# Kernel tuning notes

Measured on AMD Instinct MI355X. Metric: run time of the kernel, lower is better.

Reference implementation:

```python
import jax, jax.numpy as jnp
import numpy as np
from jax import lax

COND, PRED, DH, NOUT = 64, 32, 128, 1
M, LQ, N, LR = 8, 256, 64, 512


def setup_inputs() -> dict:
    key = jax.random.key(0)
    ks = jax.random.split(key, 8)
    g = lambda k, sh, s=0.05: jax.random.normal(k, sh, jnp.float32) * s
    return {
        "query": jax.random.normal(ks[0], (M, LQ), jnp.float32),
        "ref": jax.random.normal(ks[1], (N, LR), jnp.float32),
        "q_weight": g(ks[2], (DH, 1, COND)),
        "q_bias": jnp.zeros((DH,), jnp.float32),
        "k_weight": g(ks[3], (DH, 1, COND)),
        "k_bias": jnp.zeros((DH,), jnp.float32),
        "v_weight": g(ks[4], (DH, 1, PRED), 0.1),
        "v_bias": jnp.zeros((DH,), jnp.float32),
        "m_weight": jnp.full((NOUT, 1, COND), 1.0 / COND, jnp.float32),
        "m_bias": jnp.zeros((NOUT,), jnp.float32),
        "o_weight": g(ks[5], (NOUT * PRED, DH), 0.1),
        "o_bias": jnp.zeros((NOUT * PRED,), jnp.float32),
        "m_key": g(ks[6], (1, 1, DH), 1.0),
    }


DN = ('NCH', 'OIH', 'NCH')


def _minmax_conv(x, w, b, offset=None, scale=None):
    # x: [B,1,L], w: [H,1,k] -> y: [B,H,W]. Each length-k window is min-max
    # normalized before the conv contraction. Since offset/scale are constant
    # per window: conv((x-off)/sc) = (conv(x) - off*sum(w)) / sc.
    k = w.shape[-1]
    if offset is None:
        offset = lax.reduce_window(x, jnp.inf, lax.min, (1, 1, k), (1, 1, 1), 'VALID')
    if scale is None:
        mx = lax.reduce_window(x, -jnp.inf, lax.max, (1, 1, k), (1, 1, 1), 'VALID')
        scale = mx - offset
        scale = jnp.where(scale == 0.0, 1.0, scale)
    raw = lax.conv_general_dilated(x, w, (1,), 'VALID', dimension_numbers=DN)
    wsum = w.sum(axis=(1, 2))
    y = (raw - offset * wsum[None, :, None]) / scale + b[None, :, None]
    return y, offset, scale


def reference(query, ref, q_weight, q_bias, k_weight, k_bias, v_weight, v_bias,
              m_weight, m_bias, o_weight, o_bias, m_key):
    cond, pred = q_weight.shape[-1], v_weight.shape[-1]
    # ---- query encoding ----
    q_in = jnp.cumsum(query, axis=1)[:, None, :]
    q, q_off, q_scale = _minmax_conv(q_in, q_weight, q_bias)
    q = q.transpose(0, 2, 1)                   # [M,Q,H]
    Qn = q.shape[1]
    q_scale_t = q_scale.transpose(0, 2, 1)     # [M,Q,1]
    qp = jnp.pad(query, ((0, 0), (cond - 1, 0)))[:, None, :]
    mc = lax.conv_general_dilated(qp, m_weight, (1,), 'VALID', dimension_numbers=DN)
    mc = mc + m_bias[None, :, None]
    mc = mc[..., cond - pred:]                 # [M,NOUT,Q+pred-1]
    widx = jnp.arange(pred)[:, None] + jnp.arange(Qn)[None, :]
    mwin = mc[..., widx]                       # [M,NOUT,pred,Q]
    m = mwin.reshape(mwin.shape[0], -1, Qn).transpose(0, 2, 1)  # [M,Q,NOUT*pred]
    m = m / q_scale_t
    # ---- key / value encoding ----
    k_in = jnp.cumsum(ref, axis=1)[:, None, :-pred]
    k, k_off, k_scale = _minmax_conv(k_in, k_weight, k_bias)
    k = k.transpose(0, 2, 1)                   # [N,K,H]
    v_in = ref[:, None, cond:]
    v, _, _ = _minmax_conv(v_in, v_weight, v_bias,
                           offset=jnp.zeros_like(k_off), scale=k_scale)
    v = v.transpose(0, 2, 1)                   # [N,K,H]
    # ---- scores ----
    full_score = jnp.einsum('mqh,nkh->mqkn', q, k)           # [M,Q,K,N]
    m_score = jnp.sum(q * m_key, axis=-1, keepdims=True)     # [M,Q,1]
    # ---- semi-hard attention: top-1 window per reference series ----
    ref_score = full_score.max(axis=2)         # [M,Q,N]
    max_idx = full_score.argmax(axis=2)        # [M,Q,N]
    n_ids = jnp.arange(v.shape[0])[None, None, :]
    sel_v = v[n_ids, max_idx]                  # [M,Q,N,H]
    sel_v = sel_v @ o_weight.T + o_bias        # [M,Q,N,D]
    scores = jax.nn.softmax(jnp.concatenate([ref_score, m_score], axis=-1), axis=-1)
    rs, ms = scores[..., :-1], scores[..., -1:]
    p = jnp.einsum('mqn,mqnd->mqd', rs, sel_v) + ms * m      # [M,Q,D]
    return p * q_scale_t
```

## Files before the change

### kernel.cpp

```cpp
#include <hip/hip_runtime.h>
#include <cmath>

#define M_B   8
#define LQ    256
#define N_B   64
#define LR    512
#define COND  64
#define PRED  32
#define DH    128
#define QN    193
#define KN    417
#define QPAD  256
#define KPAD  448

typedef _Float16 half8 __attribute__((ext_vector_type(8)));
typedef float f32x16 __attribute__((ext_vector_type(16)));

__device__ __forceinline__ f32x16 mfma_f16(half8 a, half8 b, f32x16 c) {
    return __builtin_amdgcn_mfma_f32_32x32x16_f16(a, b, c, 0, 0, 0);
}
__device__ __forceinline__ f32x16 zero16() {
    f32x16 z;
    #pragma unroll
    for (int i = 0; i < 16; i++) z[i] = 0.f;
    return z;
}

#define GLOAD_LDS16(g, l) __builtin_amdgcn_global_load_lds( \
    (const __attribute__((address_space(1))) void*)(g), \
    (__attribute__((address_space(3))) void*)(l), 16, 0, 0)

__global__ void k0_scan(const float* __restrict__ q, const float* __restrict__ r,
                        float* cs_q, float* cs_r, float* mc,
                        float* q_off, float* q_scale, float* k_off, float* k_scale,
                        const float* __restrict__ mw, const float* __restrict__ mb) {
    __shared__ float x[512];
    __shared__ float s[512];
    __shared__ float P[256];
    int b = blockIdx.x, t = threadIdx.x;
    if (b < M_B) {
        x[t] = q[b * 256 + t];
        __syncthreads();
        s[t] = x[t];
        __syncthreads();
        for (int off = 1; off < 256; off <<= 1) {
            float v = (t >= off) ? s[t - off] : 0.f;
            __syncthreads();
            s[t] += v;
            __syncthreads();
        }
        cs_q[b * 256 + t] = s[t];
        float acc = mb[0];
        for (int j = 0; j < 64; j++) {
            int qi = t + j - 63;
            if (qi >= 0) acc += mw[j] * x[qi];
        }
        mc[b * 256 + t] = acc;
        if (t < QN) {
            float mn = s[t], mx = s[t];
            for (int j = 1; j < 64; j++) {
                float v = s[t + j];
                mn = fminf(mn, v); mx = fmaxf(mx, v);
            }
            float sc = mx - mn; if (sc == 0.f) sc = 1.f;
            q_off[b * QPAD + t] = mn;
            q_scale[b * QPAD + t] = sc;
        } else {
            q_off[b * QPAD + t] = 0.f;
            q_scale[b * QPAD + t] = 1.f;
        }
    } else {
        int n = b - M_B;
        x[t] = r[n * 512 + t];
        x[t + 256] = r[n * 512 + t + 256];
        __syncthreads();
        P[t] = x[2 * t] + x[2 * t + 1];
        __syncthreads();
        for (int off = 1; off < 256; off <<= 1) {
            float v = (t >= off) ? P[t - off] : 0.f;
            __syncthreads();
            P[t] += v;
            __syncthreads();
        }
        s[2 * t + 1] = P[t];
        s[2 * t]     = P[t] - x[2 * t + 1];
        __syncthreads();
        cs_r[n * 512 + t] = s[t];
        cs_r[n * 512 + t + 256] = s[t + 256];
        for (int p = t; p < KPAD; p += 256) {
            if (p < KN) {
                float mn = s[p], mx = s[p];
                for (int j = 1; j < 64; j++) {
                    float v = s[p + j];
                    mn = fminf(mn, v); mx = fmaxf(mx, v);
                }
                float sc = mx - mn; if (sc == 0.f) sc = 1.f;
                k_off[n * KPAD + p] = mn;
                k_scale[n * KPAD + p] = sc;
            } else {
                k_off[n * KPAD + p] = 0.f;
                k_scale[n * KPAD + p] = 1.f;
            }
        }
    }
}

__global__ void k1_qfeat(const float* __restrict__ cs_q, const float* __restrict__ q_off,
                         const float* __restrict__ q_scale,
                         const float* __restrict__ qw, const float* __restrict__ qb,
                         float* qfeat, _Float16* qg) {
    __shared__ float w[128 * 65];
    __shared__ float wsum[128];
    __shared__ float csS[80];
    __shared__ float offS[16], sclS[16];
    int m = blockIdx.x, chunk = blockIdx.y, t = threadIdx.x;
    int qbase = chunk * 16;
    for (int i = t; i < 8192; i += 256) {
        int h = i >> 6, j = i & 63;
        w[h * 65 + j] = qw[i];
    }
    if (t < 80) {
        int ci = qbase + t;
        csS[t] = (ci < 256) ? cs_q[m * 256 + ci] : 0.f;
    }
    if (t < 16) {
        int qpos = qbase + t;
        if (qpos < QN) { offS[t] = q_off[m * QPAD + qpos]; sclS[t] = q_scale[m * QPAD + qpos]; }
        else { offS[t] = 0.f; sclS[t] = 1.f; }
    }
    __syncthreads();
    if (t < 128) {
        float sm = 0.f;
        for (int j = 0; j < 64; j++) sm += w[t * 65 + j];
        wsum[t] = sm;
    }
    __syncthreads();
    int h = t & 127, ql0 = t >> 7;
    float bias = qb[h];
    int c = h >> 4, kh = (h >> 3) & 1, j5 = h & 7;
    for (int ql = ql0; ql < 16; ql += 2) {
        int qpos = qbase + ql;
        float val = 0.f;
        if (qpos < QN) {
            float raw = 0.f;
            #pragma unroll 8
            for (int j = 0; j < 64; j++) raw += w[h * 65 + j] * csS[ql + j];
            val = (raw - offS[ql] * wsum[h]) / sclS[ql] + bias;
        }
        qfeat[((size_t)m * QPAD + qpos) * 128 + h] = val;
        _Float16 hi = (_Float16)val;
        _Float16 lo = (_Float16)((val - (float)hi) * 1024.0f);
        int wv = (qpos >> 6) & 3, rr = (qpos >> 5) & 1, lr_ = qpos & 31;
        size_t fb = ((size_t)(m * 4 + wv) * 32) + (size_t)(rr * 8 + c) * 2;
        size_t li = (size_t)(kh * 32 + lr_) * 8 + j5;
        qg[fb * 512 + li] = hi;
        qg[(fb + 1) * 512 + li] = lo;
    }
}

__global__ void k2_kv(const float* __restrict__ cs_r, const float* __restrict__ ref,
                      const float* __restrict__ k_off, const float* __restrict__ k_scale,
                      const float* __restrict__ kw, const float* __restrict__ kb,
                      const float* __restrict__ vw, const float* __restrict__ vb,
                      _Float16* kg, float* vfeat) {
    __shared__ float w[128 * 65];
    __shared__ float vwS[128 * 33];
    __shared__ float wsum[128];
    __shared__ float csS[128];
    __shared__ float refS[96];
    __shared__ float koS[64], ksS[64];
    int n = blockIdx.x, chunk = blockIdx.y, t = threadIdx.x;
    int kbase = chunk * 64;
    for (int i = t; i < 8192; i += 256) { int h = i >> 6, j = i & 63; w[h * 65 + j] = kw[i]; }
    for (int i = t; i < 4096; i += 256) { int h = i >> 5, j = i & 31; vwS[h * 33 + j] = vw[i]; }
    if (t < 128) { int ci = kbase + t; csS[t] = (ci < 512) ? cs_r[n * 512 + ci] : 0.f; }
    if (t < 96)  { int ri = 64 + kbase + t; refS[t] = (ri < 512) ? ref[n * 512 + ri] : 0.f; }
    if (t < 64) {
        int kp = kbase + t;
        if (kp < KN) { koS[t] = k_off[n * KPAD + kp]; ksS[t] = k_scale[n * KPAD + kp]; }
        else { koS[t] = 0.f; ksS[t] = 1.f; }
    }
    __syncthreads();
    if (t < 128) {
        float sm = 0.f;
        for (int j = 0; j < 64; j++) sm += w[t * 65 + j];
        wsum[t] = sm;
    }
    __syncthreads();
    int h = t & 127, kl0 = t >> 7;
    float kbia = kb[h], vbia = vb[h];
    int cb = h >> 3, j5 = h & 7;
    for (int kl = kl0; kl < 64; kl += 2) {
        int kp = kbase + kl;
        float kval = 0.f, vval = 0.f;
        if (kp < KN) {
            float kraw = 0.f;
            #pragma unroll 8
            for (int j = 0; j < 64; j++) kraw += w[h * 65 + j] * csS[kl + j];
            float vraw = 0.f;
            #pragma unroll 8
            for (int j = 0; j < 32; j++) vraw += vwS[h * 33 + j] * refS[kl + j];
            float inv = 1.f / ksS[kl];
            kval = (kraw - koS[kl] * wsum[h]) * inv + kbia;
            vval = vraw * inv + vbia;
        }
        _Float16 khi = (_Float16)kval;
        _Float16 klo = (_Float16)((kval - (float)khi) * 1024.0f);
        size_t rowb = ((size_t)n * KPAD + kp) * 256;
        int sw = kp & 31;
        kg[rowb + (size_t)((cb ^ sw) * 8) + j5] = khi;
        kg[rowb + (size_t)(((16 + cb) ^ sw) * 8) + j5] = klo;
        vfeat[((size_t)n * KPAD + kp) * 128 + h] = vval;
    }
}

__launch_bounds__(256, 2)
__global__ void k3_score(const _Float16* __restrict__ qg, const _Float16* __restrict__ kg,
                         float* __restrict__ bscore, int* __restrict__ bidx) {
    __shared__ _Float16 Kbuf[2][32 * 256];
    const int blk = blockIdx.x;
    const int n = blk & 63, qt = blk >> 6;
    const int t = threadIdx.x, w = t >> 6, l = t & 63;
    const int lrow = l & 31, khalf = l >> 5;

    half8 qf[2][8][2];
    {
        const half8* qb = (const half8*)qg + (size_t)(qt * 4 + w) * 32 * 64 + l;
        #pragma unroll
        for (int r = 0; r < 2; r++)
            #pragma unroll
            for (int c = 0; c < 8; c++)
                #pragma unroll
                for (int h = 0; h < 2; h++)
                    qf[r][c][h] = qb[((r * 8 + c) * 2 + h) * 64];
    }

    const _Float16* ksrc = kg + (size_t)n * KPAD * 256;

    float best[2][16];
    unsigned bkt[4] = {0u, 0u, 0u, 0u};
    #pragma unroll
    for (int r = 0; r < 2; r++)
        #pragma unroll
        for (int g = 0; g < 16; g++) best[r][g] = -INFINITY;

    #pragma unroll
    for (int rd = 0; rd < 4; rd++) {
        int e = (rd * 4 + w) * 512 + l * 8;
        GLOAD_LDS16(ksrc + e, &Kbuf[0][0] + e);
    }

    for (int kt = 0; kt < 14; kt++) {
        __syncthreads();
        if (kt < 13) {
            const _Float16* src = ksrc + (size_t)(kt + 1) * (32 * 256);
            _Float16* dst = &Kbuf[(kt + 1) & 1][0];
            #pragma unroll
            for (int rd = 0; rd < 4; rd++) {
                int e = (rd * 4 + w) * 512 + l * 8;
                GLOAD_LDS16(src + e, dst + e);
            }
        }
        const _Float16* kb = &Kbuf[kt & 1][0];
        f32x16 accH[2], accL[2];
        accH[0] = zero16(); accH[1] = zero16();
        accL[0] = zero16(); accL[1] = zero16();
        #pragma unroll
        for (int c = 0; c < 8; c++) {
            half8 bh = *(const half8*)(kb + lrow * 256 + (((c * 2 + khalf) ^ lrow) * 8));
            half8 bl = *(const half8*)(kb + lrow * 256 + (((16 + c * 2 + khalf) ^ lrow) * 8));
            #pragma unroll
            for (int r = 0; r < 2; r++) {
                accH[r] = mfma_f16(qf[r][c][0], bh, accH[r]);
                accL[r] = mfma_f16(qf[r][c][0], bl, accL[r]);
                accL[r] = mfma_f16(qf[r][c][1], bh, accL[r]);
            }
        }
        const int kp = kt * 32 + lrow;
        const bool valid = kp < KN;
        #pragma unroll
        for (int r = 0; r < 2; r++) {
            #pragma unroll
            for (int g = 0; g < 16; g++) {
                float s = accH[r][g] + accL[r][g] * (1.0f / 1024.0f);
                if (valid && (s > best[r][g])) {
                    best[r][g] = s;
                    const int slot = r * 16 + g;
                    const unsigned sh = (unsigned)(slot & 7) * 4u;
                    bkt[slot >> 3] = (bkt[slot >> 3] & ~(0xFu << sh)) | ((unsigned)kt << sh);
                }
            }
        }
    }

    #pragma unroll
    for (int r = 0; r < 2; r++) {
        #pragma unroll
        for (int g = 0; g < 16; g++) {
            float s = best[r][g];
            const int slot = r * 16 + g;
            int ktb = (int)((bkt[slot >> 3] >> ((slot & 7) * 4)) & 0xFu);
            int kp = ktb * 32 + lrow;
            for (int msk = 1; msk < 32; msk <<= 1) {
                float os = __shfl_xor(s, msk, 64);
                int okp = __shfl_xor(kp, msk, 64);
                if (os > s || (os == s && okp < kp)) { s = os; kp = okp; }
            }
            if (lrow == 0) {
                int row = (g & 3) + 8 * (g >> 2) + 4 * khalf;
                int mq = qt * 256 + w * 64 + r * 32 + row;
                if ((mq & 255) < QN) {
                    bscore[(size_t)mq * 64 + n] = s;
                    bidx[(size_t)mq * 64 + n] = kp;
                }
            }
        }
    }
}

__global__ void k4_out(const float* __restrict__ qfeat, const float* __restrict__ vfeat,
                       const float* __restrict__ bscore, const int* __restrict__ bidx,
                       const float* __restrict__ q_scale, const float* __restrict__ mc,
                       const float* __restrict__ mkey,
                       const float* __restrict__ ow, const float* __restrict__ ob,
                       float* out) {
    __shared__ float sL[64]; __shared__ int iL[64];
    __shared__ float rsL[64];
    __shared__ float redA[128];
    __shared__ float wL[128];
    int bid = blockIdx.x, t = threadIdx.x;
    int m = bid / QN, qpos = bid - m * QN;
    int mq = m * QPAD + qpos;
    if (t < 64) { sL[t] = bscore[(size_t)mq * 64 + t]; iL[t] = bidx[(size_t)mq * 64 + t]; }
    redA[t] = qfeat[(size_t)mq * 128 + t] * mkey[t];
    __syncthreads();
    for (int off = 64; off > 0; off >>= 1) {
        if (t < off) redA[t] += redA[t + off];
        __syncthreads();
    }
    float msv = redA[0];
    __syncthreads();
    redA[t] = (t < 64) ? sL[t] : -INFINITY;
    __syncthreads();
    for (int off = 64; off > 0; off >>= 1) {
        if (t < off) redA[t] = fmaxf(redA[t], redA[t + off]);
        __syncthreads();
    }
    float mx = fmaxf(redA[0], msv);
    __syncthreads();
    float e = (t < 64) ? expf(sL[t] - mx) : 0.f;
    redA[t] = e;
    if (t < 64) rsL[t] = e;
    __syncthreads();
    for (int off = 64; off > 0; off >>= 1) {
        if (t < off) redA[t] += redA[t + off];
        __syncthreads();
    }
    float ems = expf(msv - mx);
    float inv = 1.f / (redA[0] + ems);
    float msw = ems * inv;
    __syncthreads();
    if (t < 64) rsL[t] *= inv;
    __syncthreads();
    float acc = 0.f;
    for (int nn = 0; nn < 64; nn++) {
        acc += rsL[nn] * vfeat[((size_t)nn * KPAD + iL[nn]) * 128 + t];
    }
    wL[t] = acc;
    __syncthreads();
    if (t < 32) {
        float p = 0.f;
        #pragma unroll 8
        for (int h = 0; h < 128; h++) p += wL[h] * ow[t * 128 + h];
        p += (1.f - msw) * ob[t];
        float outv = q_scale[mq] * p + msw * mc[m * 256 + 32 + qpos + t];
        out[((size_t)m * QN + qpos) * 32 + t] = outv;
    }
}

extern "C" void kernel_launch(void* const* d_in, const int* in_sizes, int n_in,
                              void* d_out, int out_size, void* d_ws, size_t ws_size,
                              hipStream_t stream) {
    const float* query = (const float*)d_in[0];
    const float* ref   = (const float*)d_in[1];
    const float* qw    = (const float*)d_in[2];
    const float* qb    = (const float*)d_in[3];
    const float* kw    = (const float*)d_in[4];
    const float* kb    = (const float*)d_in[5];
    const float* vw    = (const float*)d_in[6];
    const float* vb    = (const float*)d_in[7];
    const float* mw    = (const float*)d_in[8];
    const float* mb    = (const float*)d_in[9];
    const float* ow    = (const float*)d_in[10];
    const float* ob    = (const float*)d_in[11];
    const float* mkey  = (const float*)d_in[12];
    float* out = (float*)d_out;

    float* ws = (float*)d_ws;
    float* cs_q    = ws;
    float* cs_r    = cs_q + 2048;
    float* mc      = cs_r + 32768;
    float* q_off   = mc + 2048;
    float* q_scale = q_off + 2048;
    float* k_off   = q_scale + 2048;
    float* k_scale = k_off + 28672;
    float* qfeat   = k_scale + 28672;
    float* bscore  = qfeat + 262144;
    int*   bidx    = (int*)(bscore + 131072);
    _Float16* qg   = (_Float16*)(bscore + 262144);
    _Float16* kg   = (_Float16*)(bscore + 262144 + 262144);
    float* vfeat   = bscore + 262144 + 262144 + 3670016;

    hipLaunchKernelGGL(k0_scan, dim3(72), dim3(256), 0, stream,
                       query, ref, cs_q, cs_r, mc, q_off, q_scale, k_off, k_scale, mw, mb);
    hipLaunchKernelGGL(k1_qfeat, dim3(8, 16), dim3(256), 0, stream,
                       cs_q, q_off, q_scale, qw, qb, qfeat, qg);
    hipLaunchKernelGGL(k2_kv, dim3(64, 7), dim3(256), 0, stream,
                       cs_r, ref, k_off, k_scale, kw, kb, vw, vb, kg, vfeat);
    hipLaunchKernelGGL(k3_score, dim3(512), dim3(256), 0, stream,
                       qg, kg, bscore, bidx);
    hipLaunchKernelGGL(k4_out, dim3(QN * M_B), dim3(128), 0, stream,
                       qfeat, vfeat, bscore, bidx, q_scale, mc, mkey, ow, ob, out);
}
```

Before: 225.2 us.

## Restructure kv, score and output kernels for more parallelism and fewer syncs

Several kernels are reworked at once. k2_kv computes per-thread windows held in registers, reads weights straight from global memory, and stages results through LDS so kg and vfeat are written with vector stores; the key-weight sums move into an extra block of k0. k3_score gives each wave a single 32-row query tile, doubling the grid to 1024 blocks and raising the occupancy hint. k4_out processes four query rows per block, one per wave, and replaces LDS tree reductions with wave shuffles. The aim is to cut sync overhead, bring in more blocks and reduce register pressure, at the cost of reloading K tiles twice as often in k3.

Result: slower. 399.2 us (+77.3%).

```diff
diff --git a/kernel.cpp b/kernel.cpp
--- a/kernel.cpp
+++ b/kernel.cpp
@@ -33,11 +33,20 @@
 __global__ void k0_scan(const float* __restrict__ q, const float* __restrict__ r,
                         float* cs_q, float* cs_r, float* mc,
                         float* q_off, float* q_scale, float* k_off, float* k_scale,
-                        const float* __restrict__ mw, const float* __restrict__ mb) {
+                        const float* __restrict__ mw, const float* __restrict__ mb,
+                        const float* __restrict__ kw, float* wsum_k) {
     __shared__ float x[512];
     __shared__ float s[512];
     __shared__ float P[256];
     int b = blockIdx.x, t = threadIdx.x;
+    if (b == M_B + N_B) {
+        if (t < 128) {
+            float sm = 0.f;
+            for (int j = 0; j < 64; j++) sm += kw[t * 64 + j];
+            wsum_k[t] = sm;
+        }
+        return;
+    }
     if (b < M_B) {
         x[t] = q[b * 256 + t];
         __syncthreads();
@@ -150,71 +159,103 @@
         qfeat[((size_t)m * QPAD + qpos) * 128 + h] = val;
         _Float16 hi = (_Float16)val;
         _Float16 lo = (_Float16)((val - (float)hi) * 1024.0f);
-        int wv = (qpos >> 6) & 3, rr = (qpos >> 5) & 1, lr_ = qpos & 31;
-        size_t fb = ((size_t)(m * 4 + wv) * 32) + (size_t)(rr * 8 + c) * 2;
-        size_t li = (size_t)(kh * 32 + lr_) * 8 + j5;
+        int grp = (m << 3) | (qpos >> 5);
+        size_t fb = ((size_t)grp * 8 + c) * 2;
+        size_t li = (size_t)(kh * 32 + (qpos & 31)) * 8 + j5;
         qg[fb * 512 + li] = hi;
         qg[(fb + 1) * 512 + li] = lo;
     }
 }
 
+__launch_bounds__(256, 3)
 __global__ void k2_kv(const float* __restrict__ cs_r, const float* __restrict__ ref,
                       const float* __restrict__ k_off, const float* __restrict__ k_scale,
                       const float* __restrict__ kw, const float* __restrict__ kb,
                       const float* __restrict__ vw, const float* __restrict__ vb,
-                      _Float16* kg, float* vfeat) {
-    __shared__ float w[128 * 65];
-    __shared__ float vwS[128 * 33];
-    __shared__ float wsum[128];
-    __shared__ float csS[128];
-    __shared__ float refS[96];
-    __shared__ float koS[64], ksS[64];
-    int n = blockIdx.x, chunk = blockIdx.y, t = threadIdx.x;
-    int kbase = chunk * 64;
-    for (int i = t; i < 8192; i += 256) { int h = i >> 6, j = i & 63; w[h * 65 + j] = kw[i]; }
-    for (int i = t; i < 4096; i += 256) { int h = i >> 5, j = i & 31; vwS[h * 33 + j] = vw[i]; }
-    if (t < 128) { int ci = kbase + t; csS[t] = (ci < 512) ? cs_r[n * 512 + ci] : 0.f; }
-    if (t < 96)  { int ri = 64 + kbase + t; refS[t] = (ri < 512) ? ref[n * 512 + ri] : 0.f; }
-    if (t < 64) {
-        int kp = kbase + t;
-        if (kp < KN) { koS[t] = k_off[n * KPAD + kp]; ksS[t] = k_scale[n * KPAD + kp]; }
-        else { koS[t] = 0.f; ksS[t] = 1.f; }
-    }
-    __syncthreads();
-    if (t < 128) {
-        float sm = 0.f;
-        for (int j = 0; j < 64; j++) sm += w[t * 65 + j];
-        wsum[t] = sm;
-    }
-    __syncthreads();
-    int h = t & 127, kl0 = t >> 7;
-    float kbia = kb[h], vbia = vb[h];
-    int cb = h >> 3, j5 = h & 7;
-    for (int kl = kl0; kl < 64; kl += 2) {
-        int kp = kbase + kl;
-        float kval = 0.f, vval = 0.f;
-        if (kp < KN) {
-            float kraw = 0.f;
-            #pragma unroll 8
-            for (int j = 0; j < 64; j++) kraw += w[h * 65 + j] * csS[kl + j];
-            float vraw = 0.f;
-            #pragma unroll 8
-            for (int j = 0; j < 32; j++) vraw += vwS[h * 33 + j] * refS[kl + j];
-            float inv = 1.f / ksS[kl];
-            kval = (kraw - koS[kl] * wsum[h]) * inv + kbia;
-            vval = vraw * inv + vbia;
-        }
-        _Float16 khi = (_Float16)kval;
-        _Float16 klo = (_Float16)((kval - (float)khi) * 1024.0f);
-        size_t rowb = ((size_t)n * KPAD + kp) * 256;
-        int sw = kp & 31;
-        kg[rowb + (size_t)((cb ^ sw) * 8) + j5] = khi;
-        kg[rowb + (size_t)(((16 + cb) ^ sw) * 8) + j5] = klo;
-        vfeat[((size_t)n * KPAD + kp) * 128 + h] = vval;
-    }
-}
-
-__launch_bounds__(256, 2)
+                      const float* __restrict__ wsum_k,
+                      _Float16* __restrict__ kg, float* __restrict__ vfeat) {
+    __shared__ float buf[128 * 65];
+    const int n = blockIdx.x, chunk = blockIdx.y, t = threadIdx.x;
+    const int kl = t & 63, hq = t >> 6;
+    const int kp = chunk * 64 + kl;
+    const bool vkp = kp < KN;
+    const float ko  = k_off[n * KPAD + kp];
+    const float inv = 1.f / k_scale[n * KPAD + kp];
+
+    float csw[64];
+    #pragma unroll 16
+    for (int j = 0; j < 64; j++) csw[j] = cs_r[n * 512 + kp + j];
+
+    for (int hh = 0; hh < 32; hh++) {
+        const int h = hq * 32 + hh;
+        const float* wrow = kw + h * 64;
+        float a0 = 0.f, a1 = 0.f, a2 = 0.f, a3 = 0.f;
+        #pragma unroll
+        for (int j = 0; j < 64; j += 4) {
+            a0 = fmaf(wrow[j],     csw[j],     a0);
+            a1 = fmaf(wrow[j + 1], csw[j + 1], a1);
+            a2 = fmaf(wrow[j + 2], csw[j + 2], a2);
+            a3 = fmaf(wrow[j + 3], csw[j + 3], a3);
+        }
+        float kraw = (a0 + a1) + (a2 + a3);
+        float kval = vkp ? (kraw - ko * wsum_k[h]) * inv + kb[h] : 0.f;
+        buf[h * 65 + kl] = kval;
+    }
+    __syncthreads();
+    {
+        const size_t nb = ((size_t)n * KPAD + chunk * 64) * 256;
+        #pragma unroll
+        for (int r = 0; r < 8; r++) {
+            int task = r * 256 + t;
+            int kp_l = task >> 5, g = task & 31;
+            int cb = g & 15, lo = g >> 4;
+            half8 hv;
+            #pragma unroll
+            for (int jj = 0; jj < 8; jj++) {
+                float v = buf[(cb * 8 + jj) * 65 + kp_l];
+                _Float16 hi = (_Float16)v;
+                hv[jj] = lo ? (_Float16)((v - (float)hi) * 1024.0f) : hi;
+            }
+            *(half8*)&kg[nb + (size_t)kp_l * 256 + ((size_t)(g ^ (kp_l & 31)) << 3)] = hv;
+        }
+    }
+    __syncthreads();
+    float refw[32];
+    #pragma unroll 8
+    for (int j = 0; j < 32; j++) {
+        int ri = 64 + kp + j;
+        refw[j] = (ri < 512) ? ref[n * 512 + ri] : 0.f;
+    }
+    for (int hh = 0; hh < 32; hh++) {
+        const int h = hq * 32 + hh;
+        const float* vrow = vw + h * 32;
+        float b0 = 0.f, b1 = 0.f;
+        #pragma unroll
+        for (int j = 0; j < 32; j += 2) {
+            b0 = fmaf(vrow[j],     refw[j],     b0);
+            b1 = fmaf(vrow[j + 1], refw[j + 1], b1);
+        }
+        float vval = vkp ? (b0 + b1) * inv + vb[h] : 0.f;
+        buf[h * 65 + kl] = vval;
+    }
+    __syncthreads();
+    {
+        const size_t vb0 = ((size_t)n * KPAD + chunk * 64) * 128;
+        #pragma unroll
+        for (int r = 0; r < 8; r++) {
+            int idx = r * 256 + t;
+            int kp_l = idx >> 5, c4 = idx & 31;
+            float4 o;
+            o.x = buf[(c4 * 4 + 0) * 65 + kp_l];
+            o.y = buf[(c4 * 4 + 1) * 65 + kp_l];
+            o.z = buf[(c4 * 4 + 2) * 65 + kp_l];
+            o.w = buf[(c4 * 4 + 3) * 65 + kp_l];
+            *(float4*)&vfeat[vb0 + (size_t)kp_l * 128 + c4 * 4] = o;
+        }
+    }
+}
+
+__launch_bounds__(256, 3)
 __global__ void k3_score(const _Float16* __restrict__ qg, const _Float16* __restrict__ kg,
                          float* __restrict__ bscore, int* __restrict__ bidx) {
     __shared__ _Float16 Kbuf[2][32 * 256];
@@ -222,27 +263,24 @@
     const int n = blk & 63, qt = blk >> 6;
     const int t = threadIdx.x, w = t >> 6, l = t & 63;
     const int lrow = l & 31, khalf = l >> 5;
-
-    half8 qf[2][8][2];
+    const int grp = qt * 4 + w;
+
+    half8 qf[8][2];
     {
-        const half8* qb = (const half8*)qg + (size_t)(qt * 4 + w) * 32 * 64 + l;
-        #pragma unroll
-        for (int r = 0; r < 2; r++)
+        const half8* qb = (const half8*)qg + (size_t)grp * 16 * 64 + l;
+        #pragma unroll
+        for (int c = 0; c < 8; c++)
             #pragma unroll
-            for (int c = 0; c < 8; c++)
-                #pragma unroll
-                for (int h = 0; h < 2; h++)
-                    qf[r][c][h] = qb[((r * 8 + c) * 2 + h) * 64];
+            for (int h = 0; h < 2; h++)
+                qf[c][h] = qb[(c * 2 + h) * 64];
     }
 
     const _Float16* ksrc = kg + (size_t)n * KPAD * 256;
 
-    float best[2][16];
-    unsigned bkt[4] = {0u, 0u, 0u, 0u};
-    #pragma unroll
-    for (int r = 0; r < 2; r++)
-        #pragma unroll
-        for (int g = 0; g < 16; g++) best[r][g] = -INFINITY;
+    float best[16];
+    unsigned bkt0 = 0u, bkt1 = 0u;
+    #pragma unroll
+    for (int g = 0; g < 16; g++) best[g] = -INFINITY;
 
     #pragma unroll
     for (int rd = 0; rd < 4; rd++) {
@@ -250,6 +288,7 @@
         GLOAD_LDS16(ksrc + e, &Kbuf[0][0] + e);
     }
 
+    #pragma unroll
     for (int kt = 0; kt < 14; kt++) {
         __syncthreads();
         if (kt < 13) {
@@ -262,57 +301,49 @@
             }
         }
         const _Float16* kb = &Kbuf[kt & 1][0];
-        f32x16 accH[2], accL[2];
-        accH[0] = zero16(); accH[1] = zero16();
-        accL[0] = zero16(); accL[1] = zero16();
+        f32x16 accH = zero16(), accL = zero16();
         #pragma unroll
         for (int c = 0; c < 8; c++) {
             half8 bh = *(const half8*)(kb + lrow * 256 + (((c * 2 + khalf) ^ lrow) * 8));
             half8 bl = *(const half8*)(kb + lrow * 256 + (((16 + c * 2 + khalf) ^ lrow) * 8));
-            #pragma unroll
-            for (int r = 0; r < 2; r++) {
-                accH[r] = mfma_f16(qf[r][c][0], bh, accH[r]);
-                accL[r] = mfma_f16(qf[r][c][0], bl, accL[r]);
-                accL[r] = mfma_f16(qf[r][c][1], bh, accL[r]);
-            }
+            accH = mfma_f16(qf[c][0], bh, accH);
+            accL = mfma_f16(qf[c][0], bl, accL);
+            accL = mfma_f16(qf[c][1], bh, accL);
         }
         const int kp = kt * 32 + lrow;
         const bool valid = kp < KN;
         #pragma unroll
-        for (int r = 0; r < 2; r++) {
-            #pragma unroll
-            for (int g = 0; g < 16; g++) {
-                float s = accH[r][g] + accL[r][g] * (1.0f / 1024.0f);
-                if (valid && (s > best[r][g])) {
-                    best[r][g] = s;
-                    const int slot = r * 16 + g;
-                    const unsigned sh = (unsigned)(slot & 7) * 4u;
-                    bkt[slot >> 3] = (bkt[slot >> 3] & ~(0xFu << sh)) | ((unsigned)kt << sh);
-                }
-            }
-        }
-    }
-
-    #pragma unroll
-    for (int r = 0; r < 2; r++) {
-        #pragma unroll
         for (int g = 0; g < 16; g++) {
-            float s = best[r][g];
-            const int slot = r * 16 + g;
-            int ktb = (int)((bkt[slot >> 3] >> ((slot & 7) * 4)) & 0xFu);
-            int kp = ktb * 32 + lrow;
-            for (int msk = 1; msk < 32; msk <<= 1) {
-                float os = __shfl_xor(s, msk, 64);
-                int okp = __shfl_xor(kp, msk, 64);
-                if (os > s || (os == s && okp < kp)) { s = os; kp = okp; }
-            }
-            if (lrow == 0) {
-                int row = (g & 3) + 8 * (g >> 2) + 4 * khalf;
-                int mq = qt * 256 + w * 64 + r * 32 + row;
-                if ((mq & 255) < QN) {
-                    bscore[(size_t)mq * 64 + n] = s;
-                    bidx[(size_t)mq * 64 + n] = kp;
-                }
+            float s = fmaf(accL[g], 0.0009765625f, accH[g]);
+            bool upd = valid && (s > best[g]);
+            best[g] = upd ? s : best[g];
+            if (g < 8) {
+                unsigned nb = (bkt0 & ~(0xFu << (4 * g))) | ((unsigned)kt << (4 * g));
+                bkt0 = upd ? nb : bkt0;
+            } else {
+                unsigned nb = (bkt1 & ~(0xFu << (4 * (g - 8)))) | ((unsigned)kt << (4 * (g - 8)));
+                bkt1 = upd ? nb : bkt1;
+            }
+        }
+    }
+
+    #pragma unroll
+    for (int g = 0; g < 16; g++) {
+        float s = best[g];
+        int ktb = (g < 8) ? (int)((bkt0 >> (4 * g)) & 0xFu)
+                          : (int)((bkt1 >> (4 * (g - 8))) & 0xFu);
+        int kp = ktb * 32 + lrow;
+        for (int msk = 1; msk < 32; msk <<= 1) {
+            float os = __shfl_xor(s, msk, 64);
+            int okp = __shfl_xor(kp, msk, 64);
+            if (os > s || (os == s && okp < kp)) { s = os; kp = okp; }
+        }
+        if (lrow == 0) {
+            int row = (g & 3) + 8 * (g >> 2) + 4 * khalf;
+            int mq = grp * 32 + row;
+            if ((mq & 255) < QN) {
+                bscore[(size_t)mq * 64 + n] = s;
+                bidx[(size_t)mq * 64 + n] = kp;
             }
         }
     }
@@ -323,58 +354,57 @@
                        const float* __restrict__ q_scale, const float* __restrict__ mc,
                        const float* __restrict__ mkey,
                        const float* __restrict__ ow, const float* __restrict__ ob,
-                       float* out) {
-    __shared__ float sL[64]; __shared__ int iL[64];
-    __shared__ float rsL[64];
-    __shared__ float redA[128];
-    __shared__ float wL[128];
-    int bid = blockIdx.x, t = threadIdx.x;
-    int m = bid / QN, qpos = bid - m * QN;
-    int mq = m * QPAD + qpos;
-    if (t < 64) { sL[t] = bscore[(size_t)mq * 64 + t]; iL[t] = bidx[(size_t)mq * 64 + t]; }
-    redA[t] = qfeat[(size_t)mq * 128 + t] * mkey[t];
-    __syncthreads();
-    for (int off = 64; off > 0; off >>= 1) {
-        if (t < off) redA[t] += redA[t + off];
-        __syncthreads();
-    }
-    float msv = redA[0];
-    __syncthreads();
-    redA[t] = (t < 64) ? sL[t] : -INFINITY;
-    __syncthreads();
-    for (int off = 64; off > 0; off >>= 1) {
-        if (t < off) redA[t] = fmaxf(redA[t], redA[t + off]);
-        __syncthreads();
-    }
-    float mx = fmaxf(redA[0], msv);
-    __syncthreads();
-    float e = (t < 64) ? expf(sL[t] - mx) : 0.f;
-    redA[t] = e;
-    if (t < 64) rsL[t] = e;
-    __syncthreads();
-    for (int off = 64; off > 0; off >>= 1) {
-        if (t < off) redA[t] += redA[t + off];
-        __syncthreads();
-    }
+                       float* __restrict__ out) {
+    __shared__ float rsS[4][64];
+    __shared__ int   idxS[4][64];
+    __shared__ float wS[4][128];
+    const int t = threadIdx.x, wv = t >> 6, l = t & 63;
+    const int j = blockIdx.x * 4 + wv;
+    const int m = j / QN, qpos = j - m * QN;
+    const int mq = m * QPAD + qpos;
+
+    float s = bscore[(size_t)mq * 64 + l];
+    int idx = bidx[(size_t)mq * 64 + l];
+    float msv = qfeat[(size_t)mq * 128 + l] * mkey[l]
+              + qfeat[(size_t)mq * 128 + 64 + l] * mkey[64 + l];
+    #pragma unroll
+    for (int msk = 1; msk < 64; msk <<= 1) msv += __shfl_xor(msv, msk, 64);
+    float mx = s;
+    #pragma unroll
+    for (int msk = 1; msk < 64; msk <<= 1) mx = fmaxf(mx, __shfl_xor(mx, msk, 64));
+    mx = fmaxf(mx, msv);
+    float e = expf(s - mx);
+    float sum = e;
+    #pragma unroll
+    for (int msk = 1; msk < 64; msk <<= 1) sum += __shfl_xor(sum, msk, 64);
     float ems = expf(msv - mx);
-    float inv = 1.f / (redA[0] + ems);
-    float msw = ems * inv;
-    __syncthreads();
-    if (t < 64) rsL[t] *= inv;
-    __syncthreads();
-    float acc = 0.f;
+    float inv = 1.f / (sum + ems);
+    float rs = e * inv, msw = ems * inv;
+
+    rsS[wv][l] = rs; idxS[wv][l] = idx;
+    __syncthreads();
+    float ax = 0.f, ay = 0.f;
+    #pragma unroll 8
     for (int nn = 0; nn < 64; nn++) {
-        acc += rsL[nn] * vfeat[((size_t)nn * KPAD + iL[nn]) * 128 + t];
-    }
-    wL[t] = acc;
-    __syncthreads();
-    if (t < 32) {
+        float r = rsS[wv][nn];
+        int id = idxS[wv][nn];
+        const float2 v = *(const float2*)&vfeat[((size_t)nn * KPAD + id) * 128 + 2 * l];
+        ax = fmaf(r, v.x, ax);
+        ay = fmaf(r, v.y, ay);
+    }
+    wS[wv][2 * l] = ax; wS[wv][2 * l + 1] = ay;
+    __syncthreads();
+    if (l < 32) {
         float p = 0.f;
-        #pragma unroll 8
-        for (int h = 0; h < 128; h++) p += wL[h] * ow[t * 128 + h];
-        p += (1.f - msw) * ob[t];
-        float outv = q_scale[mq] * p + msw * mc[m * 256 + 32 + qpos + t];
-        out[((size_t)m * QN + qpos) * 32 + t] = outv;
+        #pragma unroll
+        for (int h4 = 0; h4 < 32; h4++) {
+            const float4 wv4 = *(const float4*)&wS[wv][h4 * 4];
+            const float4 o4 = *(const float4*)&ow[l * 128 + h4 * 4];
+            p += wv4.x * o4.x + wv4.y * o4.y + wv4.z * o4.z + wv4.w * o4.w;
+        }
+        p += (1.f - msw) * ob[l];
+        float outv = q_scale[mq] * p + msw * mc[m * 256 + 32 + qpos + l];
+        out[(size_t)j * 32 + l] = outv;
     }
 }
 
@@ -407,18 +437,20 @@
     float* qfeat   = k_scale + 28672;
     float* bscore  = qfeat + 262144;
     int*   bidx    = (int*)(bscore + 131072);
-    _Float16* qg   = (_Float16*)(bscore + 262144);
-    _Float16* kg   = (_Float16*)(bscore + 262144 + 262144);
-    float* vfeat   = bscore + 262144 + 262144 + 3670016;
-
-    hipLaunchKernelGGL(k0_scan, dim3(72), dim3(256), 0, stream,
-                       query, ref, cs_q, cs_r, mc, q_off, q_scale, k_off, k_scale, mw, mb);
+    float* wsum_k  = bscore + 262144;
+    _Float16* qg   = (_Float16*)(wsum_k + 128);
+    _Float16* kg   = (_Float16*)(wsum_k + 128 + 262144);
+    float* vfeat   = wsum_k + 128 + 262144 + 3670016;
+
+    hipLaunchKernelGGL(k0_scan, dim3(M_B + N_B + 1), dim3(256), 0, stream,
+                       query, ref, cs_q, cs_r, mc, q_off, q_scale, k_off, k_scale,
+                       mw, mb, kw, wsum_k);
     hipLaunchKernelGGL(k1_qfeat, dim3(8, 16), dim3(256), 0, stream,
                        cs_q, q_off, q_scale, qw, qb, qfeat, qg);
     hipLaunchKernelGGL(k2_kv, dim3(64, 7), dim3(256), 0, stream,
-                       cs_r, ref, k_off, k_scale, kw, kb, vw, vb, kg, vfeat);
-    hipLaunchKernelGGL(k3_score, dim3(512), dim3(256), 0, stream,
+                       cs_r, ref, k_off, k_scale, kw, kb, vw, vb, wsum_k, kg, vfeat);
+    hipLaunchKernelGGL(k3_score, dim3(1024), dim3(256), 0, stream,
                        qg, kg, bscore, bidx);
-    hipLaunchKernelGGL(k4_out, dim3(QN * M_B), dim3(128), 0, stream,
+    hipLaunchKernelGGL(k4_out, dim3(386), dim3(256), 0, stream,
                        qfeat, vfeat, bscore, bidx, q_scale, mc, mkey, ow, ob, out);
 }
```
